# Kernel tuning notes

Hardware: AMD Instinct MI355X
Metric: run time of the kernel (lower is better)

## Reference

```python
import jax, jax.numpy as jnp
import numpy as np

N_TOKENS = 18 * 24 * 24  # 10368, hard-coded in the original module


def setup_inputs() -> dict:
    key = jax.random.key(0)
    k0, k1, k2, k3, k4 = jax.random.split(key, 5)
    c = 256
    features = jax.random.normal(k0, (1, c, 18, 24, 24), dtype=jnp.float32)
    # 1x1x1 Conv3d == per-voxel linear map: weight [c//2, c], bias [c//2]
    Wi = jax.random.normal(k1, (c // 2, c), dtype=jnp.float32) * 0.05
    bi = jax.random.normal(k2, (c // 2,), dtype=jnp.float32) * 0.05
    Wj = jax.random.normal(k3, (c // 2, c), dtype=jnp.float32) * 0.05
    bj = jax.random.normal(k4, (c // 2,), dtype=jnp.float32) * 0.05
    return {"features": features, "Wi": Wi, "bi": bi, "Wj": Wj, "bj": bj}


def reference(features, Wi, bi, Wj, bj):
    # features: [1, c, 18, 24, 24]
    B, c, D, H, W = features.shape
    N = D * H * W  # 10368
    feat = features.reshape(c, N)            # [c, N] (batch == 1)
    fi = (Wi @ feat + bi[:, None]).T          # [N, c//2] (permute(1,2,3,0).view)
    fj = Wj @ feat + bj[:, None]              # [c//2, N]
    fk = feat.T                               # [N, c]
    attn = (fi @ fj) / N_TOKENS               # explicit [N, N] score matrix
    out = features + (attn @ fk).T.reshape(features.shape)
    return out
```

## Files before the change

### kernel.cpp

```cpp
#include <hip/hip_runtime.h>
#include <hip/hip_bf16.h>

#define C 256
#define C2 128
#define NTOK 10368
#define NCHUNK 36
#define KSTEPS 9
#define NTILE32 324

typedef __bf16 bf16x8 __attribute__((ext_vector_type(8)));
typedef float  f32x4  __attribute__((ext_vector_type(4)));

#define WS_Q      0
#define WS_PT     256
#define WS_SPART  33024
#define WS_FEATB  115968
#define WS_FEATT  1443072
#define WS_GPART  2770176

__device__ __constant__ int TRI_I[10] = {0,0,0,0,1,1,1,2,2,3};
__device__ __constant__ int TRI_J[10] = {0,1,2,3,1,2,3,2,3,3};

__global__ __launch_bounds__(256) void k_prep(const float* __restrict__ feat,
                                              __bf16* __restrict__ featB,
                                              __bf16* __restrict__ featT,
                                              float* __restrict__ sPart) {
    __shared__ __align__(16) ushort Ls[32][C];
    int n0 = blockIdx.x * 32;
    int c = threadIdx.x;

    float vals[32];
    float ssum = 0.f;
#pragma unroll
    for (int i = 0; i < 8; ++i) {
        float4 v = *(const float4*)(feat + (size_t)c * NTOK + n0 + i * 4);
        vals[i * 4 + 0] = v.x; vals[i * 4 + 1] = v.y;
        vals[i * 4 + 2] = v.z; vals[i * 4 + 3] = v.w;
        ssum += v.x + v.y + v.z + v.w;
    }
    sPart[blockIdx.x * C + c] = ssum;

    ushort tmp[32];
#pragma unroll
    for (int n = 0; n < 32; ++n) {
        __bf16 b = (__bf16)vals[n];
        tmp[n] = *(ushort*)&b;
        Ls[n][c] = tmp[n];
    }
    uint4* bdst = (uint4*)(featB + (size_t)c * NTOK + n0);
#pragma unroll
    for (int i = 0; i < 4; ++i) bdst[i] = ((const uint4*)tmp)[i];

    __syncthreads();
    int n = threadIdx.x >> 3;
    int koff = (threadIdx.x & 7) * 32;
    const uint4* src = (const uint4*)&Ls[n][koff];
    uint4* dst = (uint4*)(featT + (size_t)(n0 + n) * C + koff);
#pragma unroll
    for (int i = 0; i < 4; ++i) dst[i] = src[i];
}

__global__ __launch_bounds__(256) void k_gram(const __bf16* __restrict__ featB,
                                              float* __restrict__ Gpart) {
    int it = TRI_I[blockIdx.x], jt = TRI_J[blockIdx.x];
    int nc = blockIdx.y;
    int tid = threadIdx.x;
    int wave = tid >> 6, lane = tid & 63;
    int l15 = lane & 15, lq = lane >> 4;

    int i_row = it * 64 + wave * 16 + l15;
    const __bf16* fA = featB + (size_t)i_row * NTOK;
    int nbase = nc * (KSTEPS * 32);

    f32x4 acc[4];
#pragma unroll
    for (int f = 0; f < 4; ++f) acc[f] = (f32x4){0.f, 0.f, 0.f, 0.f};

#pragma unroll
    for (int ks = 0; ks < KSTEPS; ++ks) {
        int n0 = nbase + ks * 32 + lq * 8;
        bf16x8 afrag = *(const bf16x8*)(fA + n0);
#pragma unroll
        for (int f = 0; f < 4; ++f) {
            bf16x8 bfrag = *(const bf16x8*)(featB + (size_t)(jt * 64 + f * 16 + l15) * NTOK + n0);
            acc[f] = __builtin_amdgcn_mfma_f32_16x16x32_bf16(afrag, bfrag, acc[f], 0, 0, 0);
        }
    }

    float* Gp = Gpart + (size_t)nc * (C * C);
    int gib = it * 64 + wave * 16 + lq * 4;
#pragma unroll
    for (int f = 0; f < 4; ++f) {
        int gj = jt * 64 + f * 16 + l15;
#pragma unroll
        for (int r = 0; r < 4; ++r) Gp[(gib + r) * C + gj] = acc[f][r];
        if (it != jt) {
            float4 v = make_float4(acc[f][0], acc[f][1], acc[f][2], acc[f][3]);
            *(float4*)(Gp + (size_t)gj * C + gib) = v;
        }
    }
}

__global__ __launch_bounds__(256) void k_mid(const float* __restrict__ Gpart,
                                             const float* __restrict__ sPart,
                                             const float* __restrict__ Wi,
                                             const float* __restrict__ bi,
                                             const float* __restrict__ Wj,
                                             const float* __restrict__ bj,
                                             __bf16* __restrict__ Pt,
                                             float* __restrict__ q) {
    __shared__ float Gcol[C];
    __shared__ float Mpart[C];
    __shared__ float Mcol[C2];
    __shared__ float sred[8];
    int c = blockIdx.x, t = threadIdx.x;

    float g = 0.f;
    const float* gp = Gpart + (size_t)c * C + t;
#pragma unroll 4
    for (int p = 0; p < NCHUNK; ++p) g += gp[(size_t)p * (C * C)];
    Gcol[t] = g;

    float sv = 0.f;
    for (int p = t; p < NTILE32; p += 256) sv += sPart[p * C + c];
    for (int off = 32; off > 0; off >>= 1) sv += __shfl_xor(sv, off);
    if ((t & 63) == 0) sred[t >> 6] = sv;
    __syncthreads();
    float s_c = sred[0] + sred[1] + sred[2] + sred[3];

    int m = t & 127, h = t >> 7;
    float a = 0.f;
#pragma unroll 8
    for (int k0 = h * 128; k0 < h * 128 + 128; k0 += 4) {
        float4 w = *(const float4*)(Wj + m * C + k0);
        a += w.x * Gcol[k0] + w.y * Gcol[k0 + 1] + w.z * Gcol[k0 + 2] + w.w * Gcol[k0 + 3];
    }
    Mpart[t] = a;
    __syncthreads();
    if (t < C2) Mcol[t] = Mpart[t] + Mpart[t + 128] + bj[t] * s_c;
    __syncthreads();

    float acc = 0.f;
#pragma unroll 8
    for (int mm = 0; mm < C2; ++mm) acc += Wi[mm * C + t] * Mcol[mm];
    Pt[(size_t)c * C + t] = (__bf16)(acc * (1.0f / NTOK));

    float qv = (t < C2) ? bi[t] * Mcol[t] : 0.f;
    for (int off = 32; off > 0; off >>= 1) qv += __shfl_xor(qv, off);
    if ((t & 63) == 0) sred[4 + (t >> 6)] = qv;
    __syncthreads();
    if (t == 0) q[c] = (sred[4] + sred[5] + sred[6] + sred[7]) * (1.0f / NTOK);
}

__global__ __launch_bounds__(256) void k_final(const __bf16* __restrict__ featB,
                                               const __bf16* __restrict__ featT,
                                               const __bf16* __restrict__ Pt,
                                               const float* __restrict__ q,
                                               float* __restrict__ out) {
    int n0 = blockIdx.x * 32;
    int cbase = blockIdx.y * 128;
    int tid = threadIdx.x;
    int wave = tid >> 6, lane = tid & 63;
    int l15 = lane & 15, lq = lane >> 4;

    f32x4 acc[2][2];
#pragma unroll
    for (int si = 0; si < 2; ++si)
#pragma unroll
        for (int ns = 0; ns < 2; ++ns) acc[si][ns] = (f32x4){0.f, 0.f, 0.f, 0.f};

#pragma unroll
    for (int ks = 0; ks < 8; ++ks) {
        int k0 = ks * 32;
        bf16x8 b[2];
#pragma unroll
        for (int ns = 0; ns < 2; ++ns)
            b[ns] = *(const bf16x8*)(featT + (size_t)(n0 + ns * 16 + l15) * C + k0 + lq * 8);
#pragma unroll
        for (int si = 0; si < 2; ++si) {
            int crow = cbase + wave * 32 + si * 16 + l15;
            bf16x8 a = *(const bf16x8*)(Pt + (size_t)crow * C + k0 + lq * 8);
#pragma unroll
            for (int ns = 0; ns < 2; ++ns)
                acc[si][ns] = __builtin_amdgcn_mfma_f32_16x16x32_bf16(a, b[ns], acc[si][ns], 0, 0, 0);
        }
    }

#pragma unroll
    for (int si = 0; si < 2; ++si)
#pragma unroll
        for (int ns = 0; ns < 2; ++ns)
#pragma unroll
            for (int r = 0; r < 4; ++r) {
                int c = cbase + wave * 32 + si * 16 + lq * 4 + r;
                int n = n0 + ns * 16 + l15;
                float res = (float)featB[(size_t)c * NTOK + n];
                out[(size_t)c * NTOK + n] = res + q[c] + acc[si][ns][r];
            }
}

extern "C" void kernel_launch(void* const* d_in, const int* in_sizes, int n_in,
                              void* d_out, int out_size, void* d_ws, size_t ws_size,
                              hipStream_t stream) {
    const float* feat = (const float*)d_in[0];
    const float* Wi   = (const float*)d_in[1];
    const float* bi   = (const float*)d_in[2];
    const float* Wj   = (const float*)d_in[3];
    const float* bj   = (const float*)d_in[4];
    float* out = (float*)d_out;

    float* ws = (float*)d_ws;
    float*  q     = ws + WS_Q;
    __bf16* Pt    = (__bf16*)(ws + WS_PT);
    float*  sPart = ws + WS_SPART;
    __bf16* featB = (__bf16*)(ws + WS_FEATB);
    __bf16* featT = (__bf16*)(ws + WS_FEATT);
    float*  Gpart = ws + WS_GPART;

    k_prep <<<NTILE32, 256, 0, stream>>>(feat, featB, featT, sPart);
    k_gram <<<dim3(10, NCHUNK), 256, 0, stream>>>(featB, Gpart);
    k_mid  <<<256, 256, 0, stream>>>(Gpart, sPart, Wi, bi, Wj, bj, Pt, q);
    k_final<<<dim3(NTILE32, 2), 256, 0, stream>>>(featB, featT, Pt, q, out);
}
```

Baseline: 119.9 us.

## Fuse four kernels into one cooperative kernel with grid syncs and identity-folded residual

Merges the prep, Gram, mid and final kernels into a single cooperative kernel separated by grid-wide syncs, removing inter-kernel launch gaps. The residual is folded into the projection matrix by adding the identity on its diagonal, so the final phase no longer reads the bf16 feature copy. The final phase is retiled so each block covers all 256 channels for its 32 tokens. Grid syncs add barrier cost, and occupancy is constrained by the cooperative grid size.

```diff
diff --git a/kernel.cpp b/kernel.cpp
--- a/kernel.cpp
+++ b/kernel.cpp
@@ -1,5 +1,8 @@
 #include <hip/hip_runtime.h>
 #include <hip/hip_bf16.h>
+#include <hip/hip_cooperative_groups.h>
+
+namespace cg = cooperative_groups;
 
 #define C 256
 #define C2 128
@@ -7,6 +10,7 @@
 #define NCHUNK 36
 #define KSTEPS 9
 #define NTILE32 324
+#define GRID 512
 
 typedef __bf16 bf16x8 __attribute__((ext_vector_type(8)));
 typedef float  f32x4  __attribute__((ext_vector_type(4)));
@@ -21,182 +25,184 @@
 __device__ __constant__ int TRI_I[10] = {0,0,0,0,1,1,1,2,2,3};
 __device__ __constant__ int TRI_J[10] = {0,1,2,3,1,2,3,2,3,3};
 
-__global__ __launch_bounds__(256) void k_prep(const float* __restrict__ feat,
-                                              __bf16* __restrict__ featB,
-                                              __bf16* __restrict__ featT,
-                                              float* __restrict__ sPart) {
-    __shared__ __align__(16) ushort Ls[32][C];
-    int n0 = blockIdx.x * 32;
-    int c = threadIdx.x;
-
-    float vals[32];
-    float ssum = 0.f;
-#pragma unroll
-    for (int i = 0; i < 8; ++i) {
-        float4 v = *(const float4*)(feat + (size_t)c * NTOK + n0 + i * 4);
-        vals[i * 4 + 0] = v.x; vals[i * 4 + 1] = v.y;
-        vals[i * 4 + 2] = v.z; vals[i * 4 + 3] = v.w;
-        ssum += v.x + v.y + v.z + v.w;
-    }
-    sPart[blockIdx.x * C + c] = ssum;
-
-    ushort tmp[32];
-#pragma unroll
-    for (int n = 0; n < 32; ++n) {
-        __bf16 b = (__bf16)vals[n];
-        tmp[n] = *(ushort*)&b;
-        Ls[n][c] = tmp[n];
-    }
-    uint4* bdst = (uint4*)(featB + (size_t)c * NTOK + n0);
-#pragma unroll
-    for (int i = 0; i < 4; ++i) bdst[i] = ((const uint4*)tmp)[i];
-
-    __syncthreads();
-    int n = threadIdx.x >> 3;
-    int koff = (threadIdx.x & 7) * 32;
-    const uint4* src = (const uint4*)&Ls[n][koff];
-    uint4* dst = (uint4*)(featT + (size_t)(n0 + n) * C + koff);
-#pragma unroll
-    for (int i = 0; i < 4; ++i) dst[i] = src[i];
-}
-
-__global__ __launch_bounds__(256) void k_gram(const __bf16* __restrict__ featB,
-                                              float* __restrict__ Gpart) {
-    int it = TRI_I[blockIdx.x], jt = TRI_J[blockIdx.x];
-    int nc = blockIdx.y;
-    int tid = threadIdx.x;
-    int wave = tid >> 6, lane = tid & 63;
-    int l15 = lane & 15, lq = lane >> 4;
-
-    int i_row = it * 64 + wave * 16 + l15;
-    const __bf16* fA = featB + (size_t)i_row * NTOK;
-    int nbase = nc * (KSTEPS * 32);
-
-    f32x4 acc[4];
-#pragma unroll
-    for (int f = 0; f < 4; ++f) acc[f] = (f32x4){0.f, 0.f, 0.f, 0.f};
-
-#pragma unroll
-    for (int ks = 0; ks < KSTEPS; ++ks) {
-        int n0 = nbase + ks * 32 + lq * 8;
-        bf16x8 afrag = *(const bf16x8*)(fA + n0);
+__global__ __launch_bounds__(256, 2) void k_mega(const float* __restrict__ feat,
+                                                 const float* __restrict__ Wi,
+                                                 const float* __restrict__ bi,
+                                                 const float* __restrict__ Wj,
+                                                 const float* __restrict__ bj,
+                                                 float* __restrict__ out,
+                                                 __bf16* __restrict__ featB,
+                                                 __bf16* __restrict__ featT,
+                                                 float* __restrict__ sPart,
+                                                 float* __restrict__ Gpart,
+                                                 __bf16* __restrict__ Pt,
+                                                 float* __restrict__ q) {
+    cg::grid_group grid = cg::this_grid();
+    __shared__ __align__(16) char smem[16384];
+
+    const int bid = blockIdx.x;
+    const int t = threadIdx.x;
+    const int wave = t >> 6, lane = t & 63;
+    const int l15 = lane & 15, lq = lane >> 4;
+
+    if (bid < NTILE32) {
+        ushort (*Ls)[C] = (ushort (*)[C])smem;
+        int n0 = bid * 32;
+        int c = t;
+
+        float vals[32];
+        float ssum = 0.f;
+#pragma unroll
+        for (int i = 0; i < 8; ++i) {
+            float4 v = *(const float4*)(feat + (size_t)c * NTOK + n0 + i * 4);
+            vals[i * 4 + 0] = v.x; vals[i * 4 + 1] = v.y;
+            vals[i * 4 + 2] = v.z; vals[i * 4 + 3] = v.w;
+            ssum += v.x + v.y + v.z + v.w;
+        }
+        sPart[bid * C + c] = ssum;
+
+        ushort tmp[32];
+#pragma unroll
+        for (int n = 0; n < 32; ++n) {
+            __bf16 b = (__bf16)vals[n];
+            tmp[n] = *(ushort*)&b;
+            Ls[n][c] = tmp[n];
+        }
+        uint4* bdst = (uint4*)(featB + (size_t)c * NTOK + n0);
+#pragma unroll
+        for (int i = 0; i < 4; ++i) bdst[i] = ((const uint4*)tmp)[i];
+
+        __syncthreads();
+        int n = t >> 3;
+        int koff = (t & 7) * 32;
+        const uint4* src = (const uint4*)&Ls[n][koff];
+        uint4* dst = (uint4*)(featT + (size_t)(n0 + n) * C + koff);
+#pragma unroll
+        for (int i = 0; i < 4; ++i) dst[i] = src[i];
+    }
+    grid.sync();
+
+    if (bid < 10 * NCHUNK) {
+        int tri = bid / NCHUNK, nc = bid - tri * NCHUNK;
+        int it = TRI_I[tri], jt = TRI_J[tri];
+
+        int i_row = it * 64 + wave * 16 + l15;
+        const __bf16* fA = featB + (size_t)i_row * NTOK;
+        int nbase = nc * (KSTEPS * 32);
+
+        f32x4 acc[4];
+#pragma unroll
+        for (int f = 0; f < 4; ++f) acc[f] = (f32x4){0.f, 0.f, 0.f, 0.f};
+
+#pragma unroll
+        for (int ks = 0; ks < KSTEPS; ++ks) {
+            int n0 = nbase + ks * 32 + lq * 8;
+            bf16x8 afrag = *(const bf16x8*)(fA + n0);
+#pragma unroll
+            for (int f = 0; f < 4; ++f) {
+                bf16x8 bfrag = *(const bf16x8*)(featB + (size_t)(jt * 64 + f * 16 + l15) * NTOK + n0);
+                acc[f] = __builtin_amdgcn_mfma_f32_16x16x32_bf16(afrag, bfrag, acc[f], 0, 0, 0);
+            }
+        }
+
+        float* Gp = Gpart + (size_t)nc * (C * C);
+        int gib = it * 64 + wave * 16 + lq * 4;
 #pragma unroll
         for (int f = 0; f < 4; ++f) {
-            bf16x8 bfrag = *(const bf16x8*)(featB + (size_t)(jt * 64 + f * 16 + l15) * NTOK + n0);
-            acc[f] = __builtin_amdgcn_mfma_f32_16x16x32_bf16(afrag, bfrag, acc[f], 0, 0, 0);
-        }
-    }
-
-    float* Gp = Gpart + (size_t)nc * (C * C);
-    int gib = it * 64 + wave * 16 + lq * 4;
-#pragma unroll
-    for (int f = 0; f < 4; ++f) {
-        int gj = jt * 64 + f * 16 + l15;
-#pragma unroll
-        for (int r = 0; r < 4; ++r) Gp[(gib + r) * C + gj] = acc[f][r];
-        if (it != jt) {
-            float4 v = make_float4(acc[f][0], acc[f][1], acc[f][2], acc[f][3]);
-            *(float4*)(Gp + (size_t)gj * C + gib) = v;
-        }
-    }
-}
-
-__global__ __launch_bounds__(256) void k_mid(const float* __restrict__ Gpart,
-                                             const float* __restrict__ sPart,
-                                             const float* __restrict__ Wi,
-                                             const float* __restrict__ bi,
-                                             const float* __restrict__ Wj,
-                                             const float* __restrict__ bj,
-                                             __bf16* __restrict__ Pt,
-                                             float* __restrict__ q) {
-    __shared__ float Gcol[C];
-    __shared__ float Mpart[C];
-    __shared__ float Mcol[C2];
-    __shared__ float sred[8];
-    int c = blockIdx.x, t = threadIdx.x;
-
-    float g = 0.f;
-    const float* gp = Gpart + (size_t)c * C + t;
+            int gj = jt * 64 + f * 16 + l15;
+#pragma unroll
+            for (int r = 0; r < 4; ++r) Gp[(gib + r) * C + gj] = acc[f][r];
+            if (it != jt) {
+                float4 v = make_float4(acc[f][0], acc[f][1], acc[f][2], acc[f][3]);
+                *(float4*)(Gp + (size_t)gj * C + gib) = v;
+            }
+        }
+    }
+    grid.sync();
+
+    if (bid < C) {
+        float* Gcol  = (float*)smem;
+        float* Mpart = Gcol + C;
+        float* Mcol  = Mpart + C;
+        float* sred  = Mcol + C2;
+        int c = bid;
+
+        float g = 0.f;
+        const float* gp = Gpart + (size_t)c * C + t;
 #pragma unroll 4
-    for (int p = 0; p < NCHUNK; ++p) g += gp[(size_t)p * (C * C)];
-    Gcol[t] = g;
-
-    float sv = 0.f;
-    for (int p = t; p < NTILE32; p += 256) sv += sPart[p * C + c];
-    for (int off = 32; off > 0; off >>= 1) sv += __shfl_xor(sv, off);
-    if ((t & 63) == 0) sred[t >> 6] = sv;
-    __syncthreads();
-    float s_c = sred[0] + sred[1] + sred[2] + sred[3];
-
-    int m = t & 127, h = t >> 7;
-    float a = 0.f;
+        for (int p = 0; p < NCHUNK; ++p) g += gp[(size_t)p * (C * C)];
+        Gcol[t] = g;
+
+        float sv = 0.f;
+        for (int p = t; p < NTILE32; p += 256) sv += sPart[p * C + c];
+        for (int off = 32; off > 0; off >>= 1) sv += __shfl_xor(sv, off);
+        if ((t & 63) == 0) sred[t >> 6] = sv;
+        __syncthreads();
+        float s_c = sred[0] + sred[1] + sred[2] + sred[3];
+
+        int m = t & 127, h = t >> 7;
+        float a = 0.f;
 #pragma unroll 8
-    for (int k0 = h * 128; k0 < h * 128 + 128; k0 += 4) {
-        float4 w = *(const float4*)(Wj + m * C + k0);
-        a += w.x * Gcol[k0] + w.y * Gcol[k0 + 1] + w.z * Gcol[k0 + 2] + w.w * Gcol[k0 + 3];
-    }
-    Mpart[t] = a;
-    __syncthreads();
-    if (t < C2) Mcol[t] = Mpart[t] + Mpart[t + 128] + bj[t] * s_c;
-    __syncthreads();
-
-    float acc = 0.f;
+        for (int k0 = h * 128; k0 < h * 128 + 128; k0 += 4) {
+            float4 w = *(const float4*)(Wj + m * C + k0);
+            a += w.x * Gcol[k0] + w.y * Gcol[k0 + 1] + w.z * Gcol[k0 + 2] + w.w * Gcol[k0 + 3];
+        }
+        Mpart[t] = a;
+        __syncthreads();
+        if (t < C2) Mcol[t] = Mpart[t] + Mpart[t + 128] + bj[t] * s_c;
+        __syncthreads();
+
+        float acc = 0.f;
 #pragma unroll 8
-    for (int mm = 0; mm < C2; ++mm) acc += Wi[mm * C + t] * Mcol[mm];
-    Pt[(size_t)c * C + t] = (__bf16)(acc * (1.0f / NTOK));
-
-    float qv = (t < C2) ? bi[t] * Mcol[t] : 0.f;
-    for (int off = 32; off > 0; off >>= 1) qv += __shfl_xor(qv, off);
-    if ((t & 63) == 0) sred[4 + (t >> 6)] = qv;
-    __syncthreads();
-    if (t == 0) q[c] = (sred[4] + sred[5] + sred[6] + sred[7]) * (1.0f / NTOK);
-}
-
-__global__ __launch_bounds__(256) void k_final(const __bf16* __restrict__ featB,
-                                               const __bf16* __restrict__ featT,
-                                               const __bf16* __restrict__ Pt,
-                                               const float* __restrict__ q,
-                                               float* __restrict__ out) {
-    int n0 = blockIdx.x * 32;
-    int cbase = blockIdx.y * 128;
-    int tid = threadIdx.x;
-    int wave = tid >> 6, lane = tid & 63;
-    int l15 = lane & 15, lq = lane >> 4;
-
-    f32x4 acc[2][2];
-#pragma unroll
-    for (int si = 0; si < 2; ++si)
-#pragma unroll
-        for (int ns = 0; ns < 2; ++ns) acc[si][ns] = (f32x4){0.f, 0.f, 0.f, 0.f};
-
-#pragma unroll
-    for (int ks = 0; ks < 8; ++ks) {
-        int k0 = ks * 32;
-        bf16x8 b[2];
-#pragma unroll
-        for (int ns = 0; ns < 2; ++ns)
-            b[ns] = *(const bf16x8*)(featT + (size_t)(n0 + ns * 16 + l15) * C + k0 + lq * 8);
-#pragma unroll
-        for (int si = 0; si < 2; ++si) {
-            int crow = cbase + wave * 32 + si * 16 + l15;
-            bf16x8 a = *(const bf16x8*)(Pt + (size_t)crow * C + k0 + lq * 8);
+        for (int mm = 0; mm < C2; ++mm) acc += Wi[mm * C + t] * Mcol[mm];
+        float pv = acc * (1.0f / NTOK) + ((t == c) ? 1.0f : 0.0f);
+        Pt[(size_t)c * C + t] = (__bf16)pv;
+
+        float qv = (t < C2) ? bi[t] * Mcol[t] : 0.f;
+        for (int off = 32; off > 0; off >>= 1) qv += __shfl_xor(qv, off);
+        if ((t & 63) == 0) sred[4 + (t >> 6)] = qv;
+        __syncthreads();
+        if (t == 0) q[c] = (sred[4] + sred[5] + sred[6] + sred[7]) * (1.0f / NTOK);
+    }
+    grid.sync();
+
+    if (bid < NTILE32) {
+        int n0 = bid * 32;
+
+        f32x4 acc[4][2];
+#pragma unroll
+        for (int si = 0; si < 4; ++si)
+#pragma unroll
+            for (int ns = 0; ns < 2; ++ns) acc[si][ns] = (f32x4){0.f, 0.f, 0.f, 0.f};
+
+#pragma unroll
+        for (int ks = 0; ks < 8; ++ks) {
+            int k0 = ks * 32;
+            bf16x8 b[2];
 #pragma unroll
             for (int ns = 0; ns < 2; ++ns)
-                acc[si][ns] = __builtin_amdgcn_mfma_f32_16x16x32_bf16(a, b[ns], acc[si][ns], 0, 0, 0);
-        }
-    }
-
-#pragma unroll
-    for (int si = 0; si < 2; ++si)
-#pragma unroll
-        for (int ns = 0; ns < 2; ++ns)
-#pragma unroll
-            for (int r = 0; r < 4; ++r) {
-                int c = cbase + wave * 32 + si * 16 + lq * 4 + r;
-                int n = n0 + ns * 16 + l15;
-                float res = (float)featB[(size_t)c * NTOK + n];
-                out[(size_t)c * NTOK + n] = res + q[c] + acc[si][ns][r];
+                b[ns] = *(const bf16x8*)(featT + (size_t)(n0 + ns * 16 + l15) * C + k0 + lq * 8);
+#pragma unroll
+            for (int si = 0; si < 4; ++si) {
+                int crow = wave * 64 + si * 16 + l15;
+                bf16x8 a = *(const bf16x8*)(Pt + (size_t)crow * C + k0 + lq * 8);
+#pragma unroll
+                for (int ns = 0; ns < 2; ++ns)
+                    acc[si][ns] = __builtin_amdgcn_mfma_f32_16x16x32_bf16(a, b[ns], acc[si][ns], 0, 0, 0);
             }
+        }
+
+#pragma unroll
+        for (int si = 0; si < 4; ++si)
+#pragma unroll
+            for (int ns = 0; ns < 2; ++ns)
+#pragma unroll
+                for (int r = 0; r < 4; ++r) {
+                    int c = wave * 64 + si * 16 + lq * 4 + r;
+                    int n = n0 + ns * 16 + l15;
+                    out[(size_t)c * NTOK + n] = q[c] + acc[si][ns][r];
+                }
+    }
 }
 
 extern "C" void kernel_launch(void* const* d_in, const int* in_sizes, int n_in,
@@ -217,8 +223,8 @@
     __bf16* featT = (__bf16*)(ws + WS_FEATT);
     float*  Gpart = ws + WS_GPART;
 
-    k_prep <<<NTILE32, 256, 0, stream>>>(feat, featB, featT, sPart);
-    k_gram <<<dim3(10, NCHUNK), 256, 0, stream>>>(featB, Gpart);
-    k_mid  <<<256, 256, 0, stream>>>(Gpart, sPart, Wi, bi, Wj, bj, Pt, q);
-    k_final<<<dim3(NTILE32, 2), 256, 0, stream>>>(featB, featT, Pt, q, out);
+    void* args[] = {(void*)&feat, (void*)&Wi, (void*)&bi, (void*)&Wj, (void*)&bj,
+                    (void*)&out, (void*)&featB, (void*)&featT, (void*)&sPart,
+                    (void*)&Gpart, (void*)&Pt, (void*)&q};
+    hipLaunchCooperativeKernel((void*)k_mega, dim3(GRID), dim3(256), args, 0, stream);
 }
```

After: 301.1 us. 151% more time.
